# Kernel optimization log

Measured on AMD Instinct MI355X. Metric: run time of the kernel, lower is better.

## Reference

```python
import jax, jax.numpy as jnp
import numpy as np

WD, WH, WW = 7, 7, 7  # 3D window size


def _relative_position_index():
    # Matches the torch buffer construction exactly.
    coords = np.stack(np.meshgrid(np.arange(WD), np.arange(WH), np.arange(WW), indexing='ij'))  # [3,wd,wh,ww]
    cf = coords.reshape(3, -1)                      # [3, n]
    rel = cf[:, :, None] - cf[:, None, :]           # [3, n, n]
    rel = rel.transpose(1, 2, 0).copy()             # [n, n, 3]
    rel[..., 0] += WD - 1
    rel[..., 1] += WH - 1
    rel[..., 2] += WW - 1
    rel[..., 0] *= (2 * WH - 1) * (2 * WW - 1)
    rel[..., 1] *= (2 * WW - 1)
    return rel.sum(-1).astype(np.int32)             # [n, n] in [0, 2197)


def setup_inputs() -> dict:
    key = jax.random.key(0)
    ks = jax.random.split(key, 10)
    DIM, H = 192, 6
    B, N, NW = 256, WD * WH * WW, 64  # b = batch*num_windows, NW divides B
    TABLE = (2 * WD - 1) * (2 * WH - 1) * (2 * WW - 1)  # 2197
    w_std = 0.02
    mask = jnp.where(jax.random.uniform(ks[2], (NW, N, N)) < 0.1, -100.0, 0.0).astype(jnp.float32)
    return {
        'x_q': jax.random.normal(ks[0], (B, N, DIM), jnp.float32),
        'x_kv': jax.random.normal(ks[1], (B, N, DIM), jnp.float32),
        'mask': mask,
        'q_w': jax.random.normal(ks[3], (DIM, DIM), jnp.float32) * w_std,
        'q_b': jnp.zeros((DIM,), jnp.float32),
        'kv_w': jax.random.normal(ks[4], (2 * DIM, DIM), jnp.float32) * w_std,
        'kv_b': jnp.zeros((2 * DIM,), jnp.float32),
        'proj_w': jax.random.normal(ks[5], (DIM, DIM), jnp.float32) * w_std,
        'proj_b': jnp.zeros((DIM,), jnp.float32),
        'rpb_table': jax.random.normal(ks[6], (TABLE, H), jnp.float32) * w_std,
        'rpi': jnp.asarray(_relative_position_index()),
    }


def reference(x_q, x_kv, mask, q_w, q_b, kv_w, kv_b, proj_w, proj_b, rpb_table, rpi):
    b, n, c = x_q.shape
    h = rpb_table.shape[-1]
    d = c // h
    scale = d ** (-0.5)
    # projections (torch Linear: y = x @ W.T + b)
    q = (x_q @ q_w.T + q_b).reshape(b, n, h, d)
    kv = x_kv @ kv_w.T + kv_b                      # [b, n, 2c]
    k = kv[..., :c].reshape(b, n, h, d)
    v = kv[..., c:].reshape(b, n, h, d)
    # windowed QK^T
    attn = jnp.einsum('bnhd,bmhd->bhnm', q * scale, k)  # [b, h, n, n]
    # gathered relative-position bias
    rpb = rpb_table[rpi[:n, :n].reshape(-1)].reshape(n, n, h).transpose(2, 0, 1)  # [h, n, n]
    attn = attn + rpb[None]
    # window mask add
    nw = mask.shape[0]
    attn = attn.reshape(b // nw, nw, h, n, n) + mask[None, :, None]
    attn = jax.nn.softmax(attn.reshape(b, h, n, n), axis=-1)
    out = jnp.einsum('bhnm,bmhd->bnhd', attn, v).reshape(b, n, c)
    return out @ proj_w.T + proj_b
```

## Files before the change

kernel.cpp:

```cpp
#include <hip/hip_runtime.h>
#include <hip/hip_bf16.h>
#include <cstdint>

#define B_    256
#define N_    343
#define C_    192
#define H_    6
#define D_    32
#define NW_   64
#define M_    (B_*N_)
#define NN_   (N_*N_)
#define VTS_  352
#define RPS_  344
#define PBS_  376
#define SCALE_ 0.17677669529663687f
#define LOG2E_ 1.4426950408889634f
#define SCALE_LOG2E_ (SCALE_ * LOG2E_)

typedef unsigned short ushort_t;
typedef __attribute__((ext_vector_type(8))) short short8;
typedef __attribute__((ext_vector_type(4))) float f32x4;

__device__ __forceinline__ float b2f(unsigned int u) {
    return __uint_as_float(u << 16);
}
__device__ __forceinline__ unsigned int f2b(float f) {
    unsigned int x = __float_as_uint(f);
    x += 0x7FFFu + ((x >> 16) & 1u);
    return x >> 16;
}
__device__ __forceinline__ unsigned int cvt_pk(float a, float b) {
    unsigned int r;
    asm("v_cvt_pk_bf16_f32 %0, %1, %2" : "=v"(r) : "v"(a), "v"(b));
    return r;
}

__global__ __launch_bounds__(256) void wcvt(
    const float* __restrict__ qw, const float* __restrict__ kvw,
    const float* __restrict__ pw, ushort_t* __restrict__ wb)
{
    int i = blockIdx.x * 256 + threadIdx.x;
    if (i >= 36864) return;
    float4 v;
    if (i < 9216)       v = ((const float4*)qw)[i];
    else if (i < 27648) v = ((const float4*)kvw)[i - 9216];
    else                v = ((const float4*)pw)[i - 27648];
    uint2 u;
    u.x = cvt_pk(v.x, v.y);
    u.y = cvt_pk(v.z, v.w);
    ((uint2*)wb)[i] = u;
}

__global__ __launch_bounds__(512, 4) void gemm_qkv(
    const float* __restrict__ xq, const float* __restrict__ xkv,
    const ushort_t* __restrict__ wb,
    const float* __restrict__ qbias, const float* __restrict__ kvbias,
    ushort_t* __restrict__ qx, ushort_t* __restrict__ kx,
    ushort_t* __restrict__ vtb)
{
    __shared__ ushort_t wls[192 * 200];

    const int t = threadIdx.x, wv = t >> 6, lane = t & 63;
    const int quad = lane >> 4, col = lane & 15;
    const int jsel = blockIdx.y;
    const int m0 = blockIdx.x * 128;
    const ushort_t* W = wb + (size_t)jsel * 36864;
    const float* Xf = (jsel == 0) ? xq : xkv;
    const float* bias = (jsel == 0) ? qbias : (jsel == 1 ? kvbias : kvbias + 192);
    const float alpha = (jsel == 0) ? SCALE_LOG2E_ : 1.0f;

    float4 a0[6], a1[6];
    {
        const float* xp = Xf + (size_t)(m0 + wv * 16 + col) * 192;
        #pragma unroll
        for (int kt = 0; kt < 6; ++kt) {
            a0[kt] = *(const float4*)(xp + kt * 32 + quad * 8);
            a1[kt] = *(const float4*)(xp + kt * 32 + quad * 8 + 4);
        }
    }

    for (int c = t; c < 4608; c += 512) {
        int row = c / 24, off = (c % 24) * 8;
        *(short8*)(wls + row * 200 + off) = *(const short8*)(W + row * 192 + off);
    }

    short8 xf[6];
    #pragma unroll
    for (int kt = 0; kt < 6; ++kt) {
        union { short8 s; unsigned int u[4]; } f;
        f.u[0] = cvt_pk(a0[kt].x, a0[kt].y);
        f.u[1] = cvt_pk(a0[kt].z, a0[kt].w);
        f.u[2] = cvt_pk(a1[kt].x, a1[kt].y);
        f.u[3] = cvt_pk(a1[kt].z, a1[kt].w);
        xf[kt] = f.s;
    }
    __syncthreads();

    f32x4 acc[12] = {};
    #pragma unroll
    for (int kt = 0; kt < 6; ++kt)
        #pragma unroll
        for (int ct = 0; ct < 12; ++ct) {
            short8 wf = *(const short8*)(wls + (ct * 16 + col) * 200 + kt * 32 + quad * 8);
            acc[ct] = __builtin_amdgcn_mfma_f32_16x16x32_bf16(wf, xf[kt], acc[ct], 0, 0, 0);
        }

    if (jsel < 2) {
        ushort_t* o16 = (jsel == 0) ? qx : kx;
        int m = m0 + wv * 16 + col;
        int bb = m / N_, nn = m - bb * N_;
        #pragma unroll
        for (int ct = 0; ct < 12; ++ct) {
            float4 bv = *(const float4*)(bias + ct * 16 + quad * 4);
            int hh = ct >> 1;
            int dbase = (ct & 1) * 16 + quad * 4;
            float v0 = (acc[ct][0] + bv.x) * alpha;
            float v1 = (acc[ct][1] + bv.y) * alpha;
            float v2 = (acc[ct][2] + bv.z) * alpha;
            float v3 = (acc[ct][3] + bv.w) * alpha;
            uint2 pk;
            pk.x = cvt_pk(v0, v1);
            pk.y = cvt_pk(v2, v3);
            *(uint2*)(o16 + (((size_t)bb * H_ + hh) * N_ + nn) * D_ + dbase) = pk;
        }
    } else {
        int m = m0 + wv * 16 + col;
        int bb = m / N_, nn = m - bb * N_;
        #pragma unroll
        for (int ct = 0; ct < 12; ++ct) {
            float4 bv = *(const float4*)(bias + ct * 16 + quad * 4);
            int hh = ct >> 1;
            int d0 = (ct & 1) * 16 + quad * 4;
            unsigned int u01 = cvt_pk(acc[ct][0] + bv.x, acc[ct][1] + bv.y);
            unsigned int u23 = cvt_pk(acc[ct][2] + bv.z, acc[ct][3] + bv.w);
            ushort_t* vp = vtb + (((size_t)bb * H_ + hh) * D_ + d0) * VTS_ + nn;
            vp[0]            = (ushort_t)u01;
            vp[VTS_]         = (ushort_t)(u01 >> 16);
            vp[2 * VTS_]     = (ushort_t)u23;
            vp[3 * VTS_]     = (ushort_t)(u23 >> 16);
        }
    }
}

__global__ __launch_bounds__(512, 4) void gemm_out(
    const ushort_t* __restrict__ aob, const ushort_t* __restrict__ wb,
    const float* __restrict__ pbias, float* __restrict__ out)
{
    __shared__ ushort_t wls[192 * 200];

    const int t = threadIdx.x, wv = t >> 6, lane = t & 63;
    const int quad = lane >> 4, col = lane & 15;
    const int m0 = blockIdx.x * 128;
    const ushort_t* W = wb + (size_t)3 * 36864;

    short8 xf[6];
    {
        const ushort_t* xp = aob + (size_t)(m0 + wv * 16 + col) * 192;
        #pragma unroll
        for (int kt = 0; kt < 6; ++kt)
            xf[kt] = *(const short8*)(xp + kt * 32 + quad * 8);
    }
    for (int c = t; c < 4608; c += 512) {
        int row = c / 24, off = (c % 24) * 8;
        *(short8*)(wls + row * 200 + off) = *(const short8*)(W + row * 192 + off);
    }
    __syncthreads();

    f32x4 acc[12] = {};
    #pragma unroll
    for (int kt = 0; kt < 6; ++kt)
        #pragma unroll
        for (int ct = 0; ct < 12; ++ct) {
            short8 wf = *(const short8*)(wls + (ct * 16 + col) * 200 + kt * 32 + quad * 8);
            acc[ct] = __builtin_amdgcn_mfma_f32_16x16x32_bf16(wf, xf[kt], acc[ct], 0, 0, 0);
        }

    int m = m0 + wv * 16 + col;
    #pragma unroll
    for (int ct = 0; ct < 12; ++ct) {
        float4 bv = *(const float4*)(pbias + ct * 16 + quad * 4);
        float4 vo;
        vo.x = acc[ct][0] + bv.x; vo.y = acc[ct][1] + bv.y;
        vo.z = acc[ct][2] + bv.z; vo.w = acc[ct][3] + bv.w;
        *(float4*)(out + (size_t)m * 192 + ct * 16 + quad * 4) = vo;
    }
}

__global__ __launch_bounds__(256) void rpb_gather_b(
    const float* __restrict__ table, const int* __restrict__ rpi,
    ushort_t* __restrict__ rpbb)
{
    int n = blockIdx.x;
    for (int m = threadIdx.x; m < N_; m += 256) {
        int id = rpi[n * N_ + m];
        #pragma unroll
        for (int h = 0; h < H_; ++h)
            rpbb[(size_t)h * (N_ * RPS_) + (size_t)n * RPS_ + m] =
                (ushort_t)f2b(table[(size_t)id * H_ + h] * LOG2E_);
    }
}

__global__ __launch_bounds__(256) void mask_bits(
    const float* __restrict__ mask, unsigned int* __restrict__ mbits)
{
    int gw   = (blockIdx.x * 256 + threadIdx.x) >> 6;
    int lane = threadIdx.x & 63;
    int seg = gw % 6; int rem = gw / 6;
    int n = rem % N_; int w = rem / N_;
    int m = seg * 64 + lane;
    float v = (m < N_) ? mask[((size_t)w * N_ + n) * N_ + m] : -100.f;
    unsigned long long bm = __ballot(v > -50.f);
    if (lane < 2)
        mbits[((size_t)w * N_ + n) * 12 + seg * 2 + lane] = (unsigned int)(bm >> (lane * 32));
}

__global__ __launch_bounds__(256) void vt_pad(ushort_t* __restrict__ vtb)
{
    int bh = blockIdx.x;
    for (int i = threadIdx.x; i < D_ * (VTS_ - N_); i += 256) {
        int d = i / (VTS_ - N_), m = N_ + i % (VTS_ - N_);
        vtb[((size_t)bh * D_ + d) * VTS_ + m] = 0;
    }
}

__global__ __launch_bounds__(256, 2) void attn_mfma(
    const ushort_t* __restrict__ qb, const ushort_t* __restrict__ kb,
    const ushort_t* __restrict__ vtb, const ushort_t* __restrict__ rpbb,
    const unsigned int* __restrict__ mbits, ushort_t* __restrict__ aob)
{
    __shared__ ushort_t smem[24064];
    ushort_t* ks = smem;
    ushort_t* pb = smem;

    const int t = threadIdx.x, wv = t >> 6, lane = t & 63;
    const int quad = lane >> 4, col = lane & 15;
    const int qt = blockIdx.x, h = blockIdx.y, b = blockIdx.z;
    const int bh = b * H_ + h;
    const int w  = b & (NW_ - 1);
    const int n0 = qt * 64 + wv * 16;

    const ushort_t* kbase = kb + (size_t)bh * (N_ * D_);
    for (int c = t; c < (N_ * D_) / 8; c += 256) {
        int row = c >> 2, off = (c & 3) * 8;
        *(short8*)(ks + row * 40 + off) = *(const short8*)(kbase + c * 8);
    }

    int nn = n0 + col; if (nn > N_ - 1) nn = N_ - 1;
    short8 qf = *(const short8*)(qb + ((size_t)bh * N_ + nn) * D_ + quad * 8);

    const unsigned int* mbp = mbits + ((size_t)w * N_ + nn) * 12;
    uint4 mc0 = *(const uint4*)mbp;
    uint4 mc1 = *(const uint4*)(mbp + 4);
    uint4 mc2 = *(const uint4*)(mbp + 8);
    unsigned int dwv[12] = {mc0.x,mc0.y,mc0.z,mc0.w, mc1.x,mc1.y,mc1.z,mc1.w, mc2.x,mc2.y,mc2.z,mc2.w};
    const ushort_t* rpn = rpbb + (size_t)h * (N_ * RPS_) + (size_t)nn * RPS_;

    __syncthreads();

    f32x4 sacc[22];
    #pragma unroll
    for (int kt = 0; kt < 22; ++kt) {
        short8 kf = *(const short8*)(ks + (kt * 16 + col) * 40 + quad * 8);
        sacc[kt] = __builtin_amdgcn_mfma_f32_16x16x32_bf16(kf, qf, (f32x4){0.f,0.f,0.f,0.f}, 0, 0, 0);
    }
    __syncthreads();

    ushort_t* prow = pb + (size_t)(wv * 16 + col) * PBS_;
    float sum = 0.f;
    #pragma unroll
    for (int kt = 0; kt < 22; ++kt) {
        int mb4 = kt * 16 + quad * 4;
        uint2 rv = *(const uint2*)(rpn + mb4);
        unsigned int nib = (dwv[kt >> 1] >> (((kt & 1) << 4) + (quad << 2))) & 0xFu;
        float e0 = __builtin_exp2f(sacc[kt][0] + b2f(rv.x & 0xffffu));
        float e1 = __builtin_exp2f(sacc[kt][1] + b2f(rv.x >> 16));
        float e2 = __builtin_exp2f(sacc[kt][2] + b2f(rv.y & 0xffffu));
        float e3 = __builtin_exp2f(sacc[kt][3] + b2f(rv.y >> 16));
        e0 = (nib & 1u) ? e0 : 0.f;
        e1 = (nib & 2u) ? e1 : 0.f;
        e2 = (nib & 4u) ? e2 : 0.f;
        e3 = (nib & 8u) ? e3 : 0.f;
        sum += (e0 + e1) + (e2 + e3);
        uint2 pk;
        pk.x = cvt_pk(e0, e1);
        pk.y = cvt_pk(e2, e3);
        *(uint2*)(prow + kt * 16 + quad * 4) = pk;
    }
    sum += __shfl_xor(sum, 16);
    sum += __shfl_xor(sum, 32);

    const ushort_t* vbase = vtb + (size_t)bh * (D_ * VTS_);
    f32x4 oa = {0.f,0.f,0.f,0.f}, ob = {0.f,0.f,0.f,0.f};
    #pragma unroll
    for (int mt = 0; mt < 11; ++mt) {
        short8 pf = *(const short8*)(prow + mt * 32 + quad * 8);
        short8 v0 = *(const short8*)(vbase + (size_t)col * VTS_ + mt * 32 + quad * 8);
        short8 v1 = *(const short8*)(vbase + (size_t)(col + 16) * VTS_ + mt * 32 + quad * 8);
        oa = __builtin_amdgcn_mfma_f32_16x16x32_bf16(v0, pf, oa, 0, 0, 0);
        ob = __builtin_amdgcn_mfma_f32_16x16x32_bf16(v1, pf, ob, 0, 0, 0);
    }

    int n = n0 + col;
    if (n < N_) {
        float inv = 1.0f / sum;
        ushort_t* op = aob + ((size_t)b * N_ + n) * C_ + h * D_;
        uint2 p0, p1;
        p0.x = cvt_pk(oa[0] * inv, oa[1] * inv);
        p0.y = cvt_pk(oa[2] * inv, oa[3] * inv);
        p1.x = cvt_pk(ob[0] * inv, ob[1] * inv);
        p1.y = cvt_pk(ob[2] * inv, ob[3] * inv);
        *(uint2*)(op + quad * 4) = p0;
        *(uint2*)(op + 16 + quad * 4) = p1;
    }
}

extern "C" void kernel_launch(void* const* d_in, const int* in_sizes, int n_in,
                              void* d_out, int out_size, void* d_ws, size_t ws_size,
                              hipStream_t stream)
{
    const float* x_q    = (const float*)d_in[0];
    const float* x_kv   = (const float*)d_in[1];
    const float* mask   = (const float*)d_in[2];
    const float* q_w    = (const float*)d_in[3];
    const float* q_b    = (const float*)d_in[4];
    const float* kv_w   = (const float*)d_in[5];
    const float* kv_b   = (const float*)d_in[6];
    const float* proj_w = (const float*)d_in[7];
    const float* proj_b = (const float*)d_in[8];
    const float* rpb_t  = (const float*)d_in[9];
    const int*   rpi    = (const int*)d_in[10];
    float* out = (float*)d_out;

    const size_t QKV  = (size_t)B_ * H_ * N_ * D_;
    const size_t QKV2 = (size_t)B_ * H_ * D_ * VTS_;
    char* ws = (char*)d_ws;
    ushort_t* qx   = (ushort_t*)ws;
    ushort_t* kx   = qx + QKV;
    ushort_t* vtb  = kx + QKV;
    ushort_t* aob  = vtb + QKV2;
    ushort_t* rpbb = aob + QKV;
    ushort_t* wb   = rpbb + ((size_t)H_ * N_ * RPS_ + 16);
    unsigned int* mbits = (unsigned int*)(wb + 147456);

    wcvt<<<144, 256, 0, stream>>>(q_w, kv_w, proj_w, wb);
    rpb_gather_b<<<N_, 256, 0, stream>>>(rpb_t, rpi, rpbb);
    mask_bits<<<(NW_ * N_ * 6) / 4, 256, 0, stream>>>(mask, mbits);
    vt_pad<<<B_ * H_, 256, 0, stream>>>(vtb);
    gemm_qkv<<<dim3(M_/128, 3), 512, 0, stream>>>(
        x_q, x_kv, wb, q_b, kv_b, qx, kx, vtb);
    attn_mfma<<<dim3(6, H_, B_), 256, 0, stream>>>(qx, kx, vtb, rpbb, mbits, aob);
    gemm_out<<<M_/128, 512, 0, stream>>>(aob, wb, proj_b, out);
}
```

Baseline: 432.9 us.

## Stream QK-softmax-PV per tile in attention and remap blocks across XCDs

The attention kernel now processes each 32-key chunk fully (QK MFMA, bias, mask, exp, pack, then the PV MFMA) through a small per-wave LDS scratch, instead of computing all 22 score tiles first and staging a full P row buffer. This shrinks LDS use and register pressure, so the launch bound can target 5 blocks per CU instead of 2. Both the QKV GEMM and the attention kernel switch to 1D grids with an XCD-aware index remap, so neighbouring work items (the same x rows for the three projections, the same bh for the query tiles) run on the same XCD and share its L2. The interleaved loop gives the compiler less room to batch the MFMAs and adds an LDS round trip per chunk.

```diff
diff --git a/kernel.cpp b/kernel.cpp
--- a/kernel.cpp
+++ b/kernel.cpp
@@ -12,7 +12,6 @@
 #define NN_   (N_*N_)
 #define VTS_  352
 #define RPS_  344
-#define PBS_  376
 #define SCALE_ 0.17677669529663687f
 #define LOG2E_ 1.4426950408889634f
 #define SCALE_LOG2E_ (SCALE_ * LOG2E_)
@@ -62,8 +61,11 @@
 
     const int t = threadIdx.x, wv = t >> 6, lane = t & 63;
     const int quad = lane >> 4, col = lane & 15;
-    const int jsel = blockIdx.y;
-    const int m0 = blockIdx.x * 128;
+    const int lid = blockIdx.x;
+    const int xcd = lid & 7, idx = lid >> 3;
+    const int wg = (xcd < 2 ? xcd * 258 : 2 * 258 + (xcd - 2) * 257) + idx;
+    const int jsel = wg % 3;
+    const int m0 = (wg / 3) * 128;
     const ushort_t* W = wb + (size_t)jsel * 36864;
     const float* Xf = (jsel == 0) ? xq : xkv;
     const float* bias = (jsel == 0) ? qbias : (jsel == 1 ? kvbias : kvbias + 192);
@@ -223,18 +225,22 @@
     }
 }
 
-__global__ __launch_bounds__(256, 2) void attn_mfma(
+__global__ __launch_bounds__(256, 5) void attn_mfma(
     const ushort_t* __restrict__ qb, const ushort_t* __restrict__ kb,
     const ushort_t* __restrict__ vtb, const ushort_t* __restrict__ rpbb,
     const unsigned int* __restrict__ mbits, ushort_t* __restrict__ aob)
 {
-    __shared__ ushort_t smem[24064];
+    __shared__ ushort_t smem[16128];
     ushort_t* ks = smem;
-    ushort_t* pb = smem;
+    ushort_t* pbuf = smem + 14080;
 
     const int t = threadIdx.x, wv = t >> 6, lane = t & 63;
     const int quad = lane >> 4, col = lane & 15;
-    const int qt = blockIdx.x, h = blockIdx.y, b = blockIdx.z;
+    const int lid = blockIdx.x;
+    const int wg = (lid & 7) * 1152 + (lid >> 3);
+    const int qt = wg % 6;
+    const int bhx = wg / 6;
+    const int h = bhx % H_, b = bhx / H_;
     const int bh = b * H_ + h;
     const int w  = b & (NW_ - 1);
     const int n0 = qt * 64 + wv * 16;
@@ -257,48 +263,54 @@
 
     __syncthreads();
 
-    f32x4 sacc[22];
-    #pragma unroll
-    for (int kt = 0; kt < 22; ++kt) {
-        short8 kf = *(const short8*)(ks + (kt * 16 + col) * 40 + quad * 8);
-        sacc[kt] = __builtin_amdgcn_mfma_f32_16x16x32_bf16(kf, qf, (f32x4){0.f,0.f,0.f,0.f}, 0, 0, 0);
-    }
-    __syncthreads();
-
-    ushort_t* prow = pb + (size_t)(wv * 16 + col) * PBS_;
+    ushort_t* pbw = pbuf + wv * 512;
+    const ushort_t* vr0 = vtb + (size_t)bh * (D_ * VTS_) + (size_t)col * VTS_;
+    const ushort_t* vr1 = vr0 + (size_t)16 * VTS_;
+    f32x4 oa = {0.f,0.f,0.f,0.f}, ob = {0.f,0.f,0.f,0.f};
     float sum = 0.f;
-    #pragma unroll
-    for (int kt = 0; kt < 22; ++kt) {
-        int mb4 = kt * 16 + quad * 4;
-        uint2 rv = *(const uint2*)(rpn + mb4);
-        unsigned int nib = (dwv[kt >> 1] >> (((kt & 1) << 4) + (quad << 2))) & 0xFu;
-        float e0 = __builtin_exp2f(sacc[kt][0] + b2f(rv.x & 0xffffu));
-        float e1 = __builtin_exp2f(sacc[kt][1] + b2f(rv.x >> 16));
-        float e2 = __builtin_exp2f(sacc[kt][2] + b2f(rv.y & 0xffffu));
-        float e3 = __builtin_exp2f(sacc[kt][3] + b2f(rv.y >> 16));
-        e0 = (nib & 1u) ? e0 : 0.f;
-        e1 = (nib & 2u) ? e1 : 0.f;
-        e2 = (nib & 4u) ? e2 : 0.f;
-        e3 = (nib & 8u) ? e3 : 0.f;
-        sum += (e0 + e1) + (e2 + e3);
-        uint2 pk;
-        pk.x = cvt_pk(e0, e1);
-        pk.y = cvt_pk(e2, e3);
-        *(uint2*)(prow + kt * 16 + quad * 4) = pk;
-    }
+
+    #pragma unroll
+    for (int mt = 0; mt < 11; ++mt) {
+        short8 kf0 = *(const short8*)(ks + ((2*mt  ) * 16 + col) * 40 + quad * 8);
+        short8 kf1 = *(const short8*)(ks + ((2*mt+1) * 16 + col) * 40 + quad * 8);
+        f32x4 s0 = __builtin_amdgcn_mfma_f32_16x16x32_bf16(kf0, qf, (f32x4){0.f,0.f,0.f,0.f}, 0, 0, 0);
+        f32x4 s1 = __builtin_amdgcn_mfma_f32_16x16x32_bf16(kf1, qf, (f32x4){0.f,0.f,0.f,0.f}, 0, 0, 0);
+
+        uint2 rv0 = *(const uint2*)(rpn + mt * 32 + quad * 4);
+        uint2 rv1 = *(const uint2*)(rpn + mt * 32 + 16 + quad * 4);
+        unsigned int dw = dwv[mt];
+        unsigned int nib0 = (dw >> (quad << 2)) & 0xFu;
+        unsigned int nib1 = (dw >> (16 + (quad << 2))) & 0xFu;
+        float e00 = __builtin_exp2f(s0[0] + b2f(rv0.x & 0xffffu));
+        float e01 = __builtin_exp2f(s0[1] + b2f(rv0.x >> 16));
+        float e02 = __builtin_exp2f(s0[2] + b2f(rv0.y & 0xffffu));
+        float e03 = __builtin_exp2f(s0[3] + b2f(rv0.y >> 16));
+        float e10 = __builtin_exp2f(s1[0] + b2f(rv1.x & 0xffffu));
+        float e11 = __builtin_exp2f(s1[1] + b2f(rv1.x >> 16));
+        float e12 = __builtin_exp2f(s1[2] + b2f(rv1.y & 0xffffu));
+        float e13 = __builtin_exp2f(s1[3] + b2f(rv1.y >> 16));
+        e00 = (nib0 & 1u) ? e00 : 0.f;  e01 = (nib0 & 2u) ? e01 : 0.f;
+        e02 = (nib0 & 4u) ? e02 : 0.f;  e03 = (nib0 & 8u) ? e03 : 0.f;
+        e10 = (nib1 & 1u) ? e10 : 0.f;  e11 = (nib1 & 2u) ? e11 : 0.f;
+        e12 = (nib1 & 4u) ? e12 : 0.f;  e13 = (nib1 & 8u) ? e13 : 0.f;
+        sum += (e00 + e01) + (e02 + e03);
+        sum += (e10 + e11) + (e12 + e13);
+        uint2 pk0, pk1;
+        pk0.x = cvt_pk(e00, e01); pk0.y = cvt_pk(e02, e03);
+        pk1.x = cvt_pk(e10, e11); pk1.y = cvt_pk(e12, e13);
+
+        *(uint2*)(pbw + col * 32 + quad * 4)      = pk0;
+        *(uint2*)(pbw + col * 32 + 16 + quad * 4) = pk1;
+
+        short8 pf = *(const short8*)(pbw + col * 32 + quad * 8);
+        short8 v0 = *(const short8*)(vr0 + mt * 32 + quad * 8);
+        short8 v1 = *(const short8*)(vr1 + mt * 32 + quad * 8);
+        oa = __builtin_amdgcn_mfma_f32_16x16x32_bf16(v0, pf, oa, 0, 0, 0);
+        ob = __builtin_amdgcn_mfma_f32_16x16x32_bf16(v1, pf, ob, 0, 0, 0);
+    }
+
     sum += __shfl_xor(sum, 16);
     sum += __shfl_xor(sum, 32);
-
-    const ushort_t* vbase = vtb + (size_t)bh * (D_ * VTS_);
-    f32x4 oa = {0.f,0.f,0.f,0.f}, ob = {0.f,0.f,0.f,0.f};
-    #pragma unroll
-    for (int mt = 0; mt < 11; ++mt) {
-        short8 pf = *(const short8*)(prow + mt * 32 + quad * 8);
-        short8 v0 = *(const short8*)(vbase + (size_t)col * VTS_ + mt * 32 + quad * 8);
-        short8 v1 = *(const short8*)(vbase + (size_t)(col + 16) * VTS_ + mt * 32 + quad * 8);
-        oa = __builtin_amdgcn_mfma_f32_16x16x32_bf16(v0, pf, oa, 0, 0, 0);
-        ob = __builtin_amdgcn_mfma_f32_16x16x32_bf16(v1, pf, ob, 0, 0, 0);
-    }
 
     int n = n0 + col;
     if (n < N_) {
@@ -346,8 +358,8 @@
     rpb_gather_b<<<N_, 256, 0, stream>>>(rpb_t, rpi, rpbb);
     mask_bits<<<(NW_ * N_ * 6) / 4, 256, 0, stream>>>(mask, mbits);
     vt_pad<<<B_ * H_, 256, 0, stream>>>(vtb);
-    gemm_qkv<<<dim3(M_/128, 3), 512, 0, stream>>>(
+    gemm_qkv<<<2058, 512, 0, stream>>>(
         x_q, x_kv, wb, q_b, kv_b, qx, kx, vtb);
-    attn_mfma<<<dim3(6, H_, B_), 256, 0, stream>>>(qx, kx, vtb, rpbb, mbits, aob);
+    attn_mfma<<<9216, 256, 0, stream>>>(qx, kx, vtb, rpbb, mbits, aob);
     gemm_out<<<M_/128, 512, 0, stream>>>(aob, wb, proj_b, out);
 }
```

Measured after the change: 404.1 us. -6.7%, faster.

## Keep attention probabilities in registers via 32x32 MFMA and remap blocks per XCD

Applied to the files above, without the earlier changes.

The attention kernel switches from 16x16x32 to 32x32x16 MFMA tiles. Each wave now handles 32 query rows, and the bf16 probabilities are shuffled across lanes with permlane32_swap so they feed the PV MFMA directly, with no LDS round trip and no second barrier. LDS use shrinks to just the K tile, and occupancy bounds go from 2 to 5 blocks per CU. Both the QKV GEMM and attention grids are flattened and remapped so that neighbouring work lands on the same XCD for L2 reuse. The risks are more register pressure and layout assumptions in the lane swap and the hardcoded XCD partition counts.

```diff
diff --git a/kernel.cpp b/kernel.cpp
--- a/kernel.cpp
+++ b/kernel.cpp
@@ -12,7 +12,6 @@
 #define NN_   (N_*N_)
 #define VTS_  352
 #define RPS_  344
-#define PBS_  376
 #define SCALE_ 0.17677669529663687f
 #define LOG2E_ 1.4426950408889634f
 #define SCALE_LOG2E_ (SCALE_ * LOG2E_)
@@ -20,6 +19,7 @@
 typedef unsigned short ushort_t;
 typedef __attribute__((ext_vector_type(8))) short short8;
 typedef __attribute__((ext_vector_type(4))) float f32x4;
+typedef __attribute__((ext_vector_type(16))) float f32x16;
 
 __device__ __forceinline__ float b2f(unsigned int u) {
     return __uint_as_float(u << 16);
@@ -33,6 +33,9 @@
     unsigned int r;
     asm("v_cvt_pk_bf16_f32 %0, %1, %2" : "=v"(r) : "v"(a), "v"(b));
     return r;
+}
+__device__ __forceinline__ void pswap(unsigned int &x, unsigned int &y) {
+    asm("v_permlane32_swap_b32 %0, %1" : "+v"(x), "+v"(y));
 }
 
 __global__ __launch_bounds__(256) void wcvt(
@@ -62,8 +65,11 @@
 
     const int t = threadIdx.x, wv = t >> 6, lane = t & 63;
     const int quad = lane >> 4, col = lane & 15;
-    const int jsel = blockIdx.y;
-    const int m0 = blockIdx.x * 128;
+    const int lid = blockIdx.x;
+    const int xcd = lid & 7, idx = lid >> 3;
+    const int wg = (xcd < 2 ? xcd * 258 : 2 * 258 + (xcd - 2) * 257) + idx;
+    const int jsel = wg % 3;
+    const int m0 = (wg / 3) * 128;
     const ushort_t* W = wb + (size_t)jsel * 36864;
     const float* Xf = (jsel == 0) ? xq : xkv;
     const float* bias = (jsel == 0) ? qbias : (jsel == 1 ? kvbias : kvbias + 192);
@@ -223,94 +229,102 @@
     }
 }
 
-__global__ __launch_bounds__(256, 2) void attn_mfma(
+__global__ __launch_bounds__(256, 5) void attn_mfma(
     const ushort_t* __restrict__ qb, const ushort_t* __restrict__ kb,
     const ushort_t* __restrict__ vtb, const ushort_t* __restrict__ rpbb,
     const unsigned int* __restrict__ mbits, ushort_t* __restrict__ aob)
 {
-    __shared__ ushort_t smem[24064];
-    ushort_t* ks = smem;
-    ushort_t* pb = smem;
+    __shared__ ushort_t ks[352 * 40];
 
     const int t = threadIdx.x, wv = t >> 6, lane = t & 63;
-    const int quad = lane >> 4, col = lane & 15;
-    const int qt = blockIdx.x, h = blockIdx.y, b = blockIdx.z;
+    const int hh = lane >> 5, c = lane & 31;
+    const int lid = blockIdx.x;
+    const int wg = (lid & 7) * 576 + (lid >> 3);
+    const int qt = wg % 3;
+    const int bhx = wg / 3;
+    const int h = bhx % H_, b = bhx / H_;
     const int bh = b * H_ + h;
     const int w  = b & (NW_ - 1);
-    const int n0 = qt * 64 + wv * 16;
+    const int n0 = qt * 128 + wv * 32;
 
     const ushort_t* kbase = kb + (size_t)bh * (N_ * D_);
-    for (int c = t; c < (N_ * D_) / 8; c += 256) {
-        int row = c >> 2, off = (c & 3) * 8;
-        *(short8*)(ks + row * 40 + off) = *(const short8*)(kbase + c * 8);
-    }
-
-    int nn = n0 + col; if (nn > N_ - 1) nn = N_ - 1;
-    short8 qf = *(const short8*)(qb + ((size_t)bh * N_ + nn) * D_ + quad * 8);
+    for (int cc = t; cc < (N_ * D_) / 8; cc += 256) {
+        int row = cc >> 2, off = (cc & 3) * 8;
+        *(short8*)(ks + row * 40 + off) = *(const short8*)(kbase + cc * 8);
+    }
+
+    int nn = n0 + c; if (nn > N_ - 1) nn = N_ - 1;
+    const ushort_t* qp = qb + ((size_t)bh * N_ + nn) * D_;
+    short8 qf0 = *(const short8*)(qp + hh * 8);
+    short8 qf1 = *(const short8*)(qp + 16 + hh * 8);
 
     const unsigned int* mbp = mbits + ((size_t)w * N_ + nn) * 12;
     uint4 mc0 = *(const uint4*)mbp;
     uint4 mc1 = *(const uint4*)(mbp + 4);
     uint4 mc2 = *(const uint4*)(mbp + 8);
     unsigned int dwv[12] = {mc0.x,mc0.y,mc0.z,mc0.w, mc1.x,mc1.y,mc1.z,mc1.w, mc2.x,mc2.y,mc2.z,mc2.w};
-    const ushort_t* rpn = rpbb + (size_t)h * (N_ * RPS_) + (size_t)nn * RPS_;
+    const ushort_t* rpn = rpbb + (size_t)h * (N_ * RPS_) + (size_t)nn * RPS_ + hh * 4;
 
     __syncthreads();
 
-    f32x4 sacc[22];
-    #pragma unroll
-    for (int kt = 0; kt < 22; ++kt) {
-        short8 kf = *(const short8*)(ks + (kt * 16 + col) * 40 + quad * 8);
-        sacc[kt] = __builtin_amdgcn_mfma_f32_16x16x32_bf16(kf, qf, (f32x4){0.f,0.f,0.f,0.f}, 0, 0, 0);
-    }
-    __syncthreads();
-
-    ushort_t* prow = pb + (size_t)(wv * 16 + col) * PBS_;
+    const ushort_t* vbase = vtb + (size_t)bh * (D_ * VTS_) + (size_t)c * VTS_;
+    f32x16 oacc = {};
     float sum = 0.f;
-    #pragma unroll
-    for (int kt = 0; kt < 22; ++kt) {
-        int mb4 = kt * 16 + quad * 4;
-        uint2 rv = *(const uint2*)(rpn + mb4);
-        unsigned int nib = (dwv[kt >> 1] >> (((kt & 1) << 4) + (quad << 2))) & 0xFu;
-        float e0 = __builtin_exp2f(sacc[kt][0] + b2f(rv.x & 0xffffu));
-        float e1 = __builtin_exp2f(sacc[kt][1] + b2f(rv.x >> 16));
-        float e2 = __builtin_exp2f(sacc[kt][2] + b2f(rv.y & 0xffffu));
-        float e3 = __builtin_exp2f(sacc[kt][3] + b2f(rv.y >> 16));
-        e0 = (nib & 1u) ? e0 : 0.f;
-        e1 = (nib & 2u) ? e1 : 0.f;
-        e2 = (nib & 4u) ? e2 : 0.f;
-        e3 = (nib & 8u) ? e3 : 0.f;
-        sum += (e0 + e1) + (e2 + e3);
-        uint2 pk;
-        pk.x = cvt_pk(e0, e1);
-        pk.y = cvt_pk(e2, e3);
-        *(uint2*)(prow + kt * 16 + quad * 4) = pk;
-    }
-    sum += __shfl_xor(sum, 16);
+
+    #pragma unroll
+    for (int kt = 0; kt < 11; ++kt) {
+        const ushort_t* krow = ks + (kt * 32 + c) * 40 + hh * 8;
+        short8 ka = *(const short8*)(krow);
+        short8 kb2 = *(const short8*)(krow + 16);
+        f32x16 s = {};
+        s = __builtin_amdgcn_mfma_f32_32x32x16_bf16(ka,  qf0, s, 0, 0, 0);
+        s = __builtin_amdgcn_mfma_f32_32x32x16_bf16(kb2, qf1, s, 0, 0, 0);
+
+        unsigned int nibs = dwv[kt] >> (hh * 4);
+        unsigned int pk[8];
+        #pragma unroll
+        for (int g = 0; g < 4; ++g) {
+            uint2 rv = *(const uint2*)(rpn + kt * 32 + g * 8);
+            unsigned int nib = (nibs >> (g * 8)) & 0xFu;
+            float e0 = __builtin_exp2f(s[4*g+0] + b2f(rv.x & 0xffffu));
+            float e1 = __builtin_exp2f(s[4*g+1] + b2f(rv.x >> 16));
+            float e2 = __builtin_exp2f(s[4*g+2] + b2f(rv.y & 0xffffu));
+            float e3 = __builtin_exp2f(s[4*g+3] + b2f(rv.y >> 16));
+            e0 = (nib & 1u) ? e0 : 0.f;
+            e1 = (nib & 2u) ? e1 : 0.f;
+            e2 = (nib & 4u) ? e2 : 0.f;
+            e3 = (nib & 8u) ? e3 : 0.f;
+            sum += (e0 + e1) + (e2 + e3);
+            pk[2*g]   = cvt_pk(e0, e1);
+            pk[2*g+1] = cvt_pk(e2, e3);
+        }
+        pswap(pk[0], pk[2]);
+        pswap(pk[1], pk[3]);
+        pswap(pk[4], pk[6]);
+        pswap(pk[5], pk[7]);
+        union { short8 s8; unsigned int u[4]; } pf1, pf2;
+        pf1.u[0] = pk[0]; pf1.u[1] = pk[1]; pf1.u[2] = pk[2]; pf1.u[3] = pk[3];
+        pf2.u[0] = pk[4]; pf2.u[1] = pk[5]; pf2.u[2] = pk[6]; pf2.u[3] = pk[7];
+
+        short8 vf1 = *(const short8*)(vbase + kt * 32 + hh * 8);
+        short8 vf2 = *(const short8*)(vbase + kt * 32 + 16 + hh * 8);
+        oacc = __builtin_amdgcn_mfma_f32_32x32x16_bf16(vf1, pf1.s8, oacc, 0, 0, 0);
+        oacc = __builtin_amdgcn_mfma_f32_32x32x16_bf16(vf2, pf2.s8, oacc, 0, 0, 0);
+    }
+
     sum += __shfl_xor(sum, 32);
 
-    const ushort_t* vbase = vtb + (size_t)bh * (D_ * VTS_);
-    f32x4 oa = {0.f,0.f,0.f,0.f}, ob = {0.f,0.f,0.f,0.f};
-    #pragma unroll
-    for (int mt = 0; mt < 11; ++mt) {
-        short8 pf = *(const short8*)(prow + mt * 32 + quad * 8);
-        short8 v0 = *(const short8*)(vbase + (size_t)col * VTS_ + mt * 32 + quad * 8);
-        short8 v1 = *(const short8*)(vbase + (size_t)(col + 16) * VTS_ + mt * 32 + quad * 8);
-        oa = __builtin_amdgcn_mfma_f32_16x16x32_bf16(v0, pf, oa, 0, 0, 0);
-        ob = __builtin_amdgcn_mfma_f32_16x16x32_bf16(v1, pf, ob, 0, 0, 0);
-    }
-
-    int n = n0 + col;
+    int n = n0 + c;
     if (n < N_) {
         float inv = 1.0f / sum;
-        ushort_t* op = aob + ((size_t)b * N_ + n) * C_ + h * D_;
-        uint2 p0, p1;
-        p0.x = cvt_pk(oa[0] * inv, oa[1] * inv);
-        p0.y = cvt_pk(oa[2] * inv, oa[3] * inv);
-        p1.x = cvt_pk(ob[0] * inv, ob[1] * inv);
-        p1.y = cvt_pk(ob[2] * inv, ob[3] * inv);
-        *(uint2*)(op + quad * 4) = p0;
-        *(uint2*)(op + 16 + quad * 4) = p1;
+        ushort_t* op = aob + ((size_t)b * N_ + n) * C_ + h * D_ + hh * 4;
+        #pragma unroll
+        for (int g = 0; g < 4; ++g) {
+            uint2 pkk;
+            pkk.x = cvt_pk(oacc[4*g+0] * inv, oacc[4*g+1] * inv);
+            pkk.y = cvt_pk(oacc[4*g+2] * inv, oacc[4*g+3] * inv);
+            *(uint2*)(op + g * 8) = pkk;
+        }
     }
 }
 
@@ -346,8 +360,8 @@
     rpb_gather_b<<<N_, 256, 0, stream>>>(rpb_t, rpi, rpbb);
     mask_bits<<<(NW_ * N_ * 6) / 4, 256, 0, stream>>>(mask, mbits);
     vt_pad<<<B_ * H_, 256, 0, stream>>>(vtb);
-    gemm_qkv<<<dim3(M_/128, 3), 512, 0, stream>>>(
+    gemm_qkv<<<2058, 512, 0, stream>>>(
         x_q, x_kv, wb, q_b, kv_b, qx, kx, vtb);
-    attn_mfma<<<dim3(6, H_, B_), 256, 0, stream>>>(qx, kx, vtb, rpbb, mbits, aob);
+    attn_mfma<<<4608, 256, 0, stream>>>(qx, kx, vtb, rpbb, mbits, aob);
     gemm_out<<<M_/128, 512, 0, stream>>>(aob, wb, proj_b, out);
 }
```

After: 394.4 us. 8.9% less time.
